# Performance work log

Measured on AMD Instinct MI355X. Metric: run time of the kernel, lower is better.

The kernel has to match this reference:

```python
import jax, jax.numpy as jnp
import numpy as np

D_MODEL = 1024
N_HEADS = 16
D_HEAD = 64
D_FF = 4096
WINDOW = 256
B, T = 2, 2048


def setup_inputs() -> dict:
    key = jax.random.key(0)
    ks = jax.random.split(key, 10)
    tot = N_HEADS * D_HEAD
    def w(k, shape):
        # approximate kaiming_normal_ fan_out init: std = sqrt(2/fan_out)
        fan_out = shape[0]
        return jax.random.normal(k, shape, jnp.float32) * np.sqrt(2.0 / fan_out)
    return {
        "x": jax.random.normal(ks[0], (B, T, D_MODEL), jnp.float32),
        "ln1_w": jnp.ones((D_MODEL,), jnp.float32),
        "qkv_w": w(ks[1], (3 * tot, D_MODEL)),
        "gate_w": w(ks[2], (tot, D_MODEL)),
        "out_w": w(ks[3], (D_MODEL, tot)),
        "ln2_w": jnp.ones((D_MODEL,), jnp.float32),
        "wg": w(ks[4], (D_FF, D_MODEL)),
        "wu": w(ks[5], (D_FF, D_MODEL)),
        "wo": w(ks[6], (D_MODEL, D_FF)),
    }


def _rmsnorm(x, w):
    return x * jax.lax.rsqrt(jnp.mean(x * x, axis=-1, keepdims=True) + 1e-6) * w


def _attention(x, qkv_w, gate_w, out_w):
    Bq, Tq, _ = x.shape
    tot = N_HEADS * D_HEAD
    qkv = x @ qkv_w.T  # [B,T,3*tot]
    q, k, v = jnp.split(qkv, 3, axis=-1)
    q = q.reshape(Bq, Tq, N_HEADS, D_HEAD).transpose(0, 2, 1, 3)
    k = k.reshape(Bq, Tq, N_HEADS, D_HEAD).transpose(0, 2, 1, 3)
    v = v.reshape(Bq, Tq, N_HEADS, D_HEAD).transpose(0, 2, 1, 3)
    scale = D_HEAD ** -0.5
    scores = jnp.einsum("bhqd,bhkd->bhqk", q, k) * scale
    pos = jnp.arange(Tq)
    dist = pos[:, None] - pos[None, :]
    allowed = (dist >= 0) & (dist < WINDOW)  # causal sliding window
    mask = jnp.where(allowed, 0.0, -jnp.inf).astype(scores.dtype)
    attn = jax.nn.softmax(scores + mask[None, None], axis=-1)
    out = jnp.einsum("bhqk,bhkd->bhqd", attn, v)
    out = out.transpose(0, 2, 1, 3).reshape(Bq, Tq, tot)
    gate = jax.nn.sigmoid(x @ gate_w.T)
    return (out * gate) @ out_w.T


def reference(x, ln1_w, qkv_w, gate_w, out_w, ln2_w, wg, wu, wo):
    x = x + _attention(_rmsnorm(x, ln1_w), qkv_w, gate_w, out_w)
    h = _rmsnorm(x, ln2_w)
    ffn = (jax.nn.silu(h @ wg.T) * (h @ wu.T)) @ wo.T
    return x + ffn
```

## Files before the change

### kernel.cpp

```cpp
#include <hip/hip_runtime.h>


#define DEV __device__ __forceinline__

using u16 = unsigned short;
typedef __attribute__((ext_vector_type(8))) short  short8;
typedef __attribute__((ext_vector_type(4))) float  floatx4;

DEV u16 f2bf(float f) {
  unsigned u = __builtin_bit_cast(unsigned, f);
  u += 0x7FFFu + ((u >> 16) & 1u);
  return (u16)(u >> 16);
}
DEV float bf2f(u16 h) {
  unsigned u = ((unsigned)h) << 16;
  return __builtin_bit_cast(float, u);
}
DEV floatx4 mfma16(short8 a, short8 b, floatx4 c) {
  return __builtin_amdgcn_mfma_f32_16x16x32_bf16(a, b, c, 0, 0, 0);
}
DEV void gload16(const u16* g, const u16* lds_base_wave_uniform) {
  __builtin_amdgcn_global_load_lds(
      (const __attribute__((address_space(1))) void*)g,
      (__attribute__((address_space(3))) void*)lds_base_wave_uniform,
      16, 0, 0);
}
#define WAITVM(n) asm volatile("s_waitcnt vmcnt(" #n ")" ::: "memory")
DEV void blockbar() {
  __builtin_amdgcn_sched_barrier(0);
  asm volatile("" ::: "memory");
  __builtin_amdgcn_s_barrier();
  asm volatile("" ::: "memory");
  __builtin_amdgcn_sched_barrier(0);
}

__global__ __launch_bounds__(256) void cvt_all_k(
    const float* __restrict__ s0, const float* __restrict__ s1,
    const float* __restrict__ s2, const float* __restrict__ s3,
    const float* __restrict__ s4, const float* __restrict__ s5,
    u16* __restrict__ d0, u16* __restrict__ d1, u16* __restrict__ d2,
    u16* __restrict__ d3, u16* __restrict__ d4, u16* __restrict__ d5) {
  const int b = blockIdx.x;
  const float* in; u16* out; int base;
  if (b < 3072)       { in = s0; out = d0; base = 0; }
  else if (b < 4096)  { in = s1; out = d1; base = 3072; }
  else if (b < 5120)  { in = s2; out = d2; base = 4096; }
  else if (b < 9216)  { in = s3; out = d3; base = 5120; }
  else if (b < 13312) { in = s4; out = d4; base = 9216; }
  else                { in = s5; out = d5; base = 13312; }
  const size_t i = (size_t)(b - base) * 256 + threadIdx.x;
  const float4 v = ((const float4*)in)[i];
  ushort4 r;
  r.x = f2bf(v.x); r.y = f2bf(v.y); r.z = f2bf(v.z); r.w = f2bf(v.w);
  ((ushort4*)out)[i] = r;
}

__global__ __launch_bounds__(256) void rmsnorm_k(const float* __restrict__ x,
                                                 const float* __restrict__ wt,
                                                 u16* __restrict__ o) {
  __shared__ float red[4];
  const int row = blockIdx.x;
  const int tid = threadIdx.x;
  const float4 v = ((const float4*)(x + (size_t)row * 1024))[tid];
  float ss = v.x * v.x + v.y * v.y + v.z * v.z + v.w * v.w;
  ss += __shfl_xor(ss, 1, 64);
  ss += __shfl_xor(ss, 2, 64);
  ss += __shfl_xor(ss, 4, 64);
  ss += __shfl_xor(ss, 8, 64);
  ss += __shfl_xor(ss, 16, 64);
  ss += __shfl_xor(ss, 32, 64);
  if ((tid & 63) == 0) red[tid >> 6] = ss;
  __syncthreads();
  const float tot = red[0] + red[1] + red[2] + red[3];
  const float sc = rsqrtf(tot * (1.0f / 1024.0f) + 1e-6f);
  const float4 wv = ((const float4*)wt)[tid];
  ushort4 r;
  r.x = f2bf(v.x * sc * wv.x);
  r.y = f2bf(v.y * sc * wv.y);
  r.z = f2bf(v.z * sc * wv.z);
  r.w = f2bf(v.w * sc * wv.w);
  ((ushort4*)(o + (size_t)row * 1024))[tid] = r;
}

template <int CFG, int EPI>
__global__ __launch_bounds__(512, 2) void gemm8w(
    const u16* __restrict__ Ag, const u16* __restrict__ Bg, int N, int K,
    u16* __restrict__ cb, float* __restrict__ cf,
    const u16* __restrict__ aux, const float* __restrict__ resid,
    u16* __restrict__ cb2) {
  constexpr int BM = (CFG == 0) ? 256 : 128;
  constexpr int TB = BM * 64;
  constexpr int CPW = TB / 1024 / 8;
  constexpr int NI = (BM / 2) / 16;
  constexpr int NJ = (BM / 4) / 16;
  __shared__ __align__(16) char lds[8 * TB];

  const int tid = threadIdx.x;
  const int w = tid >> 6, lane = tid & 63;
  const int wm = w >> 2, wn = w & 3;
  const int g = lane >> 4, r16 = lane & 15;
  const int wr0 = wm * (BM / 2), wc0 = wn * (BM / 4);

  int bid = blockIdx.y * gridDim.x + blockIdx.x;
  const int cpx = (gridDim.x * gridDim.y) >> 3;
  bid = (bid & 7) * cpx + (bid >> 3);
  const int m0 = (bid / gridDim.x) * BM;
  const int n0 = (bid % gridDim.x) * BM;

  floatx4 acc[NI][NJ];
#pragma unroll
  for (int i = 0; i < NI; i++)
#pragma unroll
    for (int j = 0; j < NJ; j++) acc[i][j] = (floatx4){0.f, 0.f, 0.f, 0.f};

  const int nk = K >> 5;
  const int xorlane = ((lane >> 3) & 7) << 4;

  auto stage = [&](int t) {
    const int bufo = (t & 3) * TB;
    const int k0 = t << 5;
#pragma unroll
    for (int q = 0; q < CPW; ++q) {
      const int c = w + (q << 3);
      const int d = (c << 10) + (lane << 4);
      const int bl = d ^ xorlane;
      const int row = ((bl >> 7) << 1) | ((bl >> 6) & 1);
      const int col = (bl & 63) >> 1;
      gload16(Ag + (size_t)(m0 + row) * K + k0 + col,
              (const u16*)(lds + bufo + (c << 10)));
      gload16(Bg + (size_t)(n0 + row) * K + k0 + col,
              (const u16*)(lds + 4 * TB + bufo + (c << 10)));
    }
  };

  stage(0); stage(1); stage(2);
  if constexpr (CFG == 0) WAITVM(8); else WAITVM(4);
  blockbar();

  const int xorr = ((r16 >> 1) & 7) << 4;
  const int baseA = ((((wr0 + r16) >> 1) << 7) + ((r16 & 1) << 6) + (g << 4)) ^ xorr;
  const int baseB = ((((wc0 + r16) >> 1) << 7) + ((r16 & 1) << 6) + (g << 4)) ^ xorr;

  for (int kt = 0; kt < nk; ++kt) {
    if (kt + 3 < nk) stage(kt + 3);
    const char* Ab = lds + (kt & 3) * TB;
    const char* Bb = lds + 4 * TB + (kt & 3) * TB;

    short8 af[NI / 2], bfv[NJ];
#pragma unroll
    for (int q = 0; q < NI / 2; q++) af[q] = *(const short8*)(Ab + baseA + (q << 10));
#pragma unroll
    for (int q = 0; q < NJ / 2; q++) bfv[q] = *(const short8*)(Bb + baseB + (q << 10));
    __builtin_amdgcn_s_setprio(1);
#pragma unroll
    for (int i = 0; i < NI / 2; i++)
#pragma unroll
      for (int j = 0; j < NJ / 2; j++) acc[i][j] = mfma16(af[i], bfv[j], acc[i][j]);
    __builtin_amdgcn_s_setprio(0);
#pragma unroll
    for (int q = NJ / 2; q < NJ; q++) bfv[q] = *(const short8*)(Bb + baseB + (q << 10));
    __builtin_amdgcn_s_setprio(1);
#pragma unroll
    for (int i = 0; i < NI / 2; i++)
#pragma unroll
      for (int j = NJ / 2; j < NJ; j++) acc[i][j] = mfma16(af[i], bfv[j], acc[i][j]);
    __builtin_amdgcn_s_setprio(0);
#pragma unroll
    for (int q = 0; q < NI / 2; q++)
      af[q] = *(const short8*)(Ab + baseA + ((NI / 2 + q) << 10));
    __builtin_amdgcn_s_setprio(1);
#pragma unroll
    for (int i = 0; i < NI / 2; i++)
#pragma unroll
      for (int j = NJ / 2; j < NJ; j++)
        acc[NI / 2 + i][j] = mfma16(af[i], bfv[j], acc[NI / 2 + i][j]);
    __builtin_amdgcn_s_setprio(0);
    __builtin_amdgcn_s_setprio(1);
#pragma unroll
    for (int i = 0; i < NI / 2; i++)
#pragma unroll
      for (int j = 0; j < NJ / 2; j++)
        acc[NI / 2 + i][j] = mfma16(af[i], bfv[j], acc[NI / 2 + i][j]);
    __builtin_amdgcn_s_setprio(0);

    if (kt + 1 < nk) {
      if (kt + 3 < nk)      { if constexpr (CFG == 0) WAITVM(8); else WAITVM(4); }
      else if (kt + 2 < nk) { if constexpr (CFG == 0) WAITVM(4); else WAITVM(2); }
      else                  { WAITVM(0); }
      blockbar();
    }
  }

#pragma unroll
  for (int i = 0; i < NI; i++) {
    const int row = m0 + wr0 + i * 16 + g * 4;
#pragma unroll
    for (int j = 0; j < NJ; j++) {
      const int col = n0 + wc0 + j * 16 + r16;
#pragma unroll
      for (int rr = 0; rr < 4; rr++) {
        const float v = acc[i][j][rr];
        if constexpr (EPI == 2) {
          cb[(size_t)(row + rr) * N + col] = f2bf(v / (1.0f + __expf(-v)));
        } else if constexpr (EPI == 3) {
          const size_t idx = (size_t)(row + rr) * N + col;
          cb[idx] = f2bf(v * bf2f(aux[idx]));
        } else if constexpr (EPI == 4) {
          const size_t idx = (size_t)(row + rr) * N + col;
          cf[idx] = v + resid[idx];
        } else if constexpr (EPI == 6) {
          if (col < 3072)
            cb[(size_t)(row + rr) * 3072 + col] = f2bf(v);
          else
            cb2[(size_t)(row + rr) * 1024 + (col - 3072)] =
                f2bf(1.0f / (1.0f + __expf(-v)));
        }
      }
    }
  }
}

__global__ __launch_bounds__(256) void attn_win_kernel(
    const u16* __restrict__ qkv, const u16* __restrict__ gate,
    u16* __restrict__ out) {
  __shared__ __align__(16) u16 Kl[64][80];
  __shared__ __align__(16) u16 Vt[64][80];
  __shared__ __align__(16) u16 Pl[4][16][80];

  const int tid = threadIdx.x;
  const int w = tid >> 6, lane = tid & 63;
  const int g = lane >> 4, r16 = lane & 15;

  const int q0 = blockIdx.x * 64;
  const int h = blockIdx.y;
  const int b = blockIdx.z;
  const u16* qb_ = qkv + (size_t)b * 2048 * 3072;

  const int tq = q0 + w * 16 + r16;
  const u16* qptr = qb_ + (size_t)tq * 3072 + h * 64;
  const short8 aq0 = *(const short8*)(qptr + g * 8);
  const short8 aq1 = *(const short8*)(qptr + 32 + g * 8);

  floatx4 O[4] = {{0,0,0,0},{0,0,0,0},{0,0,0,0},{0,0,0,0}};
  float mrow[4] = {-1e30f, -1e30f, -1e30f, -1e30f};
  float lrow[4] = {0.f, 0.f, 0.f, 0.f};

  const int srow = tid >> 2;
  const int sq4 = tid & 3;
  const int qw = q0 + w * 16;

  for (int kt = q0 - 256; kt <= q0; kt += 64) {
    if (kt < 0) continue;
    {
      const u16* kb = qb_ + (size_t)(kt + srow) * 3072 + 1024 + h * 64 + sq4 * 16;
      const short8 kv0 = *(const short8*)kb;
      const short8 kv1 = *(const short8*)(kb + 8);
      *(short8*)&Kl[srow][sq4 * 16] = kv0;
      *(short8*)&Kl[srow][sq4 * 16 + 8] = kv1;
      const u16* vb = kb + 1024;
      const short8 vv0 = *(const short8*)vb;
      const short8 vv1 = *(const short8*)(vb + 8);
#pragma unroll
      for (int j = 0; j < 8; j++) Vt[sq4 * 16 + j][srow] = (u16)vv0[j];
#pragma unroll
      for (int j = 0; j < 8; j++) Vt[sq4 * 16 + 8 + j][srow] = (u16)vv1[j];
    }
    __syncthreads();

    const bool active = (qw + 15 >= kt) && (qw - kt < 319);
    if (active) {
      floatx4 S[4];
#pragma unroll
      for (int nf = 0; nf < 4; nf++) {
        const short8 bk0 = *(const short8*)&Kl[nf * 16 + r16][g * 8];
        const short8 bk1 = *(const short8*)&Kl[nf * 16 + r16][32 + g * 8];
        floatx4 a = {0.f, 0.f, 0.f, 0.f};
        a = mfma16(aq0, bk0, a);
        a = mfma16(aq1, bk1, a);
        S[nf] = a;
      }
      float pm[4][4];
      float nmax[4] = {-1e30f, -1e30f, -1e30f, -1e30f};
#pragma unroll
      for (int nf = 0; nf < 4; nf++) {
        const int key = kt + nf * 16 + r16;
#pragma unroll
        for (int rr = 0; rr < 4; rr++) {
          const int q = qw + g * 4 + rr;
          const int dist = q - key;
          const float s = (dist >= 0 && dist < 256) ? S[nf][rr] : -1e30f;
          pm[nf][rr] = s;
          nmax[rr] = fmaxf(nmax[rr], s);
        }
      }
#pragma unroll
      for (int rr = 0; rr < 4; rr++) {
        float v = nmax[rr];
        v = fmaxf(v, __shfl_xor(v, 1, 64));
        v = fmaxf(v, __shfl_xor(v, 2, 64));
        v = fmaxf(v, __shfl_xor(v, 4, 64));
        v = fmaxf(v, __shfl_xor(v, 8, 64));
        const float mnew = fmaxf(mrow[rr], v);
        const float alpha = __expf(0.125f * (mrow[rr] - mnew));
        mrow[rr] = mnew;
        lrow[rr] *= alpha;
#pragma unroll
        for (int n = 0; n < 4; n++) O[n][rr] *= alpha;
        float ls = 0.f;
#pragma unroll
        for (int nf = 0; nf < 4; nf++) {
          const float s = pm[nf][rr];
          const float pv = (s < -1e29f) ? 0.f : __expf(0.125f * (s - mnew));
          pm[nf][rr] = pv;
          ls += pv;
        }
        ls += __shfl_xor(ls, 1, 64);
        ls += __shfl_xor(ls, 2, 64);
        ls += __shfl_xor(ls, 4, 64);
        ls += __shfl_xor(ls, 8, 64);
        lrow[rr] += ls;
      }
#pragma unroll
      for (int nf = 0; nf < 4; nf++)
#pragma unroll
        for (int rr = 0; rr < 4; rr++)
          Pl[w][g * 4 + rr][nf * 16 + r16] = f2bf(pm[nf][rr]);
#pragma unroll
      for (int kf = 0; kf < 2; kf++) {
        const short8 pa = *(const short8*)&Pl[w][r16][kf * 32 + g * 8];
#pragma unroll
        for (int n = 0; n < 4; n++) {
          const short8 vb8 = *(const short8*)&Vt[n * 16 + r16][kf * 32 + g * 8];
          O[n] = mfma16(pa, vb8, O[n]);
        }
      }
    }
    __syncthreads();
  }

#pragma unroll
  for (int n = 0; n < 4; n++) {
#pragma unroll
    for (int rr = 0; rr < 4; rr++) {
      const int t = qw + g * 4 + rr;
      const size_t idx = ((size_t)(b * 2048 + t)) * 1024 + h * 64 + n * 16 + r16;
      const float gv = bf2f(gate[idx]);
      const float ov = (O[n][rr] / lrow[rr]) * gv;
      out[idx] = f2bf(ov);
    }
  }
}

extern "C" void kernel_launch(void* const* d_in, const int* in_sizes, int n_in,
                              void* d_out, int out_size, void* d_ws,
                              size_t ws_size, hipStream_t stream) {
  (void)in_sizes; (void)n_in; (void)out_size; (void)ws_size;
  const float* x     = (const float*)d_in[0];
  const float* ln1   = (const float*)d_in[1];
  const float* qkvw  = (const float*)d_in[2];
  const float* gatew = (const float*)d_in[3];
  const float* outw  = (const float*)d_in[4];
  const float* ln2   = (const float*)d_in[5];
  const float* wg    = (const float*)d_in[6];
  const float* wu    = (const float*)d_in[7];
  const float* wo    = (const float*)d_in[8];
  float* outp = (float*)d_out;

  u16* p = (u16*)d_ws;
  u16* qkvw_b  = p; p += 3 * 1024 * 1024;
  u16* gatew_b = p; p += 1024 * 1024;
  u16* outw_b  = p; p += 1024 * 1024;
  u16* wg_b    = p; p += 4 * 1024 * 1024;
  u16* wu_b    = p; p += 4 * 1024 * 1024;
  u16* wo_b    = p; p += 4 * 1024 * 1024;
  u16* xn      = p; p += 4096 * 1024;
  u16* qkvb    = p; p += (size_t)4096 * 3072;
  u16* gates   = p; p += 4096 * 1024;
  u16* a3      = p; p += 4096 * 1024;
  u16* hb      = p; p += 4096 * 1024;
  u16* gs      = p; p += (size_t)4096 * 4096;
  float* x2    = (float*)p;

  cvt_all_k<<<17408, 256, 0, stream>>>(qkvw, gatew, outw, wg, wu, wo,
                                       qkvw_b, gatew_b, outw_b, wg_b, wu_b, wo_b);

  rmsnorm_k<<<4096, 256, 0, stream>>>(x, ln1, xn);

  gemm8w<0, 6><<<dim3(16, 16), 512, 0, stream>>>(
      xn, qkvw_b, 4096, 1024, qkvb, nullptr, nullptr, nullptr, gates);

  attn_win_kernel<<<dim3(32, 16, 2), 256, 0, stream>>>(qkvb, gates, a3);

  gemm8w<1, 4><<<dim3(8, 32), 512, 0, stream>>>(
      a3, outw_b, 1024, 1024, nullptr, x2, nullptr, x, nullptr);

  rmsnorm_k<<<4096, 256, 0, stream>>>(x2, ln2, hb);

  gemm8w<0, 2><<<dim3(16, 16), 512, 0, stream>>>(
      hb, wg_b, 4096, 1024, gs, nullptr, nullptr, nullptr, nullptr);
  gemm8w<0, 3><<<dim3(16, 16), 512, 0, stream>>>(
      hb, wu_b, 4096, 1024, gs, nullptr, gs, nullptr, nullptr);

  gemm8w<1, 4><<<dim3(8, 32), 512, 0, stream>>>(
      gs, wo_b, 1024, 4096, nullptr, outp, nullptr, x2, nullptr);
}
```

Before: 389.0 us.

## Restructure GEMM into double-buffered 64-wide K tiles with interleaved sub-stage loads

Rewrites the bf16 MFMA GEMM pipeline. The old kernel used a 4-deep ring of 32-wide K stages with XOR-swizzled LDS. The new one uses two 64-wide K buffers split into four sub-groups (A/B by K half), whose loads for the next tile are issued between the MFMA phases of the current tile. The 128-tile configuration now runs with 4 waves (256 threads) instead of 8, each wave computing a 64x64 output. The aim is to overlap global-to-LDS traffic with compute and cut barrier overhead. The risks are that dropping the XOR swizzle adds LDS bank conflicts, and that the extra in-loop barriers and fewer waves on the small GEMMs reduce latency hiding.

```diff
diff --git a/kernel.cpp b/kernel.cpp
--- a/kernel.cpp
+++ b/kernel.cpp
@@ -19,7 +19,7 @@
 DEV floatx4 mfma16(short8 a, short8 b, floatx4 c) {
   return __builtin_amdgcn_mfma_f32_16x16x32_bf16(a, b, c, 0, 0, 0);
 }
-DEV void gload16(const u16* g, const u16* lds_base_wave_uniform) {
+DEV void gload16(const u16* g, const char* lds_base_wave_uniform) {
   __builtin_amdgcn_global_load_lds(
       (const __attribute__((address_space(1))) void*)g,
       (__attribute__((address_space(3))) void*)lds_base_wave_uniform,
@@ -27,11 +27,9 @@
 }
 #define WAITVM(n) asm volatile("s_waitcnt vmcnt(" #n ")" ::: "memory")
 DEV void blockbar() {
-  __builtin_amdgcn_sched_barrier(0);
   asm volatile("" ::: "memory");
   __builtin_amdgcn_s_barrier();
   asm volatile("" ::: "memory");
-  __builtin_amdgcn_sched_barrier(0);
 }
 
 __global__ __launch_bounds__(256) void cvt_all_k(
@@ -83,23 +81,26 @@
 }
 
 template <int CFG, int EPI>
-__global__ __launch_bounds__(512, 2) void gemm8w(
+__global__ __launch_bounds__((CFG == 0) ? 512 : 256, 2) void gemm8p(
     const u16* __restrict__ Ag, const u16* __restrict__ Bg, int N, int K,
     u16* __restrict__ cb, float* __restrict__ cf,
     const u16* __restrict__ aux, const float* __restrict__ resid,
     u16* __restrict__ cb2) {
   constexpr int BM = (CFG == 0) ? 256 : 128;
-  constexpr int TB = BM * 64;
-  constexpr int CPW = TB / 1024 / 8;
-  constexpr int NI = (BM / 2) / 16;
-  constexpr int NJ = (BM / 4) / 16;
-  __shared__ __align__(16) char lds[8 * TB];
+  constexpr int NWAVES = (CFG == 0) ? 8 : 4;
+  constexpr int WAVES_N = (CFG == 0) ? 4 : 2;
+  constexpr int WM = (CFG == 0) ? 128 : 64;
+  constexpr int NI = WM / 16;
+  constexpr int NJ = 4;
+  constexpr int IH = (CFG == 0) ? NI / 2 : NI;
+  constexpr int GB = BM * 64;
+  constexpr int BUFB = 4 * GB;
+  __shared__ __align__(16) char lds[2 * BUFB];
 
   const int tid = threadIdx.x;
   const int w = tid >> 6, lane = tid & 63;
-  const int wm = w >> 2, wn = w & 3;
+  const int wm = w / WAVES_N, wn = w % WAVES_N;
   const int g = lane >> 4, r16 = lane & 15;
-  const int wr0 = wm * (BM / 2), wc0 = wn * (BM / 4);
 
   int bid = blockIdx.y * gridDim.x + blockIdx.x;
   const int cpx = (gridDim.x * gridDim.y) >> 3;
@@ -113,90 +114,90 @@
 #pragma unroll
     for (int j = 0; j < NJ; j++) acc[i][j] = (floatx4){0.f, 0.f, 0.f, 0.f};
 
-  const int nk = K >> 5;
-  const int xorlane = ((lane >> 3) & 7) << 4;
-
-  auto stage = [&](int t) {
-    const int bufo = (t & 3) * TB;
-    const int k0 = t << 5;
-#pragma unroll
-    for (int q = 0; q < CPW; ++q) {
-      const int c = w + (q << 3);
-      const int d = (c << 10) + (lane << 4);
-      const int bl = d ^ xorlane;
-      const int row = ((bl >> 7) << 1) | ((bl >> 6) & 1);
-      const int col = (bl & 63) >> 1;
-      gload16(Ag + (size_t)(m0 + row) * K + k0 + col,
-              (const u16*)(lds + bufo + (c << 10)));
-      gload16(Bg + (size_t)(n0 + row) * K + k0 + col,
-              (const u16*)(lds + 4 * TB + bufo + (c << 10)));
-    }
+  const int nt = K >> 6;
+
+  const int srow = w * 32 + (lane >> 2);
+  const int scol8 = (lane & 3) * 8;
+  auto stageG = [&](int G, int t) {
+    if (t >= nt) return;
+    const u16* Mat = (G < 2) ? Ag : Bg;
+    const int base0 = (G < 2) ? m0 : n0;
+    const int kc = t * 64 + (G & 1) * 32 + scol8;
+    const char* dst = lds + (t & 1) * BUFB + G * GB + w * 2048;
+#pragma unroll
+    for (int q = 0; q < 2; q++)
+      gload16(Mat + (size_t)(base0 + srow + q * 16) * K + kc, dst + q * 1024);
   };
 
-  stage(0); stage(1); stage(2);
-  if constexpr (CFG == 0) WAITVM(8); else WAITVM(4);
-  blockbar();
-
-  const int xorr = ((r16 >> 1) & 7) << 4;
-  const int baseA = ((((wr0 + r16) >> 1) << 7) + ((r16 & 1) << 6) + (g << 4)) ^ xorr;
-  const int baseB = ((((wc0 + r16) >> 1) << 7) + ((r16 & 1) << 6) + (g << 4)) ^ xorr;
-
-  for (int kt = 0; kt < nk; ++kt) {
-    if (kt + 3 < nk) stage(kt + 3);
-    const char* Ab = lds + (kt & 3) * TB;
-    const char* Bb = lds + 4 * TB + (kt & 3) * TB;
-
-    short8 af[NI / 2], bfv[NJ];
-#pragma unroll
-    for (int q = 0; q < NI / 2; q++) af[q] = *(const short8*)(Ab + baseA + (q << 10));
-#pragma unroll
-    for (int q = 0; q < NJ / 2; q++) bfv[q] = *(const short8*)(Bb + baseB + (q << 10));
+  auto rdA = [&](short8* af, int ks, int ihalf, const char* buf) {
+#pragma unroll
+    for (int i = 0; i < IH; i++) {
+      const int arow = wm * WM + (ihalf * IH + i) * 16 + r16;
+      af[i] = *(const short8*)(buf + ks * GB + arow * 64 + g * 16);
+    }
+  };
+  auto rdB = [&](short8* bf_, int ks, const char* buf) {
+#pragma unroll
+    for (int j = 0; j < NJ; j++) {
+      const int brow = wn * 64 + j * 16 + r16;
+      bf_[j] = *(const short8*)(buf + 2 * GB + ks * GB + brow * 64 + g * 16);
+    }
+  };
+  auto mm = [&](short8* af, short8* bf_, int ihalf) {
     __builtin_amdgcn_s_setprio(1);
 #pragma unroll
-    for (int i = 0; i < NI / 2; i++)
-#pragma unroll
-      for (int j = 0; j < NJ / 2; j++) acc[i][j] = mfma16(af[i], bfv[j], acc[i][j]);
+    for (int i = 0; i < IH; i++)
+#pragma unroll
+      for (int j = 0; j < NJ; j++)
+        acc[ihalf * IH + i][j] = mfma16(af[i], bf_[j], acc[ihalf * IH + i][j]);
     __builtin_amdgcn_s_setprio(0);
-#pragma unroll
-    for (int q = NJ / 2; q < NJ; q++) bfv[q] = *(const short8*)(Bb + baseB + (q << 10));
-    __builtin_amdgcn_s_setprio(1);
-#pragma unroll
-    for (int i = 0; i < NI / 2; i++)
-#pragma unroll
-      for (int j = NJ / 2; j < NJ; j++) acc[i][j] = mfma16(af[i], bfv[j], acc[i][j]);
-    __builtin_amdgcn_s_setprio(0);
-#pragma unroll
-    for (int q = 0; q < NI / 2; q++)
-      af[q] = *(const short8*)(Ab + baseA + ((NI / 2 + q) << 10));
-    __builtin_amdgcn_s_setprio(1);
-#pragma unroll
-    for (int i = 0; i < NI / 2; i++)
-#pragma unroll
-      for (int j = NJ / 2; j < NJ; j++)
-        acc[NI / 2 + i][j] = mfma16(af[i], bfv[j], acc[NI / 2 + i][j]);
-    __builtin_amdgcn_s_setprio(0);
-    __builtin_amdgcn_s_setprio(1);
-#pragma unroll
-    for (int i = 0; i < NI / 2; i++)
-#pragma unroll
-      for (int j = 0; j < NJ / 2; j++)
-        acc[NI / 2 + i][j] = mfma16(af[i], bfv[j], acc[NI / 2 + i][j]);
-    __builtin_amdgcn_s_setprio(0);
-
-    if (kt + 1 < nk) {
-      if (kt + 3 < nk)      { if constexpr (CFG == 0) WAITVM(8); else WAITVM(4); }
-      else if (kt + 2 < nk) { if constexpr (CFG == 0) WAITVM(4); else WAITVM(2); }
-      else                  { WAITVM(0); }
-      blockbar();
+  };
+
+  if constexpr (CFG == 0) { stageG(1, 0); stageG(2, 0); stageG(0, 0); stageG(3, 0); }
+  else                    { stageG(0, 0); stageG(2, 0); stageG(1, 0); stageG(3, 0); }
+
+  for (int t = 0; t < nt; ++t) {
+    const char* buf = lds + (t & 1) * BUFB;
+    short8 af[IH], bfv[NJ];
+    if constexpr (CFG == 0) {
+      WAITVM(2);
+      blockbar();
+      rdA(af, 0, 0, buf); rdB(bfv, 0, buf);
+      stageG(1, t + 1);
+      mm(af, bfv, 0);
+      blockbar();
+      rdA(af, 0, 1, buf);
+      stageG(2, t + 1);
+      mm(af, bfv, 1);
+      if (t + 1 < nt) { WAITVM(4); } else { WAITVM(0); }
+      blockbar();
+      rdA(af, 1, 0, buf); rdB(bfv, 1, buf);
+      stageG(0, t + 1);
+      mm(af, bfv, 0);
+      blockbar();
+      rdA(af, 1, 1, buf);
+      stageG(3, t + 1);
+      mm(af, bfv, 1);
+    } else {
+      WAITVM(4);
+      blockbar();
+      rdA(af, 0, 0, buf); rdB(bfv, 0, buf);
+      stageG(0, t + 1); stageG(2, t + 1);
+      mm(af, bfv, 0);
+      if (t + 1 < nt) { WAITVM(4); } else { WAITVM(0); }
+      blockbar();
+      rdA(af, 1, 0, buf); rdB(bfv, 1, buf);
+      stageG(1, t + 1); stageG(3, t + 1);
+      mm(af, bfv, 0);
     }
   }
 
 #pragma unroll
   for (int i = 0; i < NI; i++) {
-    const int row = m0 + wr0 + i * 16 + g * 4;
+    const int row = m0 + wm * WM + i * 16 + g * 4;
 #pragma unroll
     for (int j = 0; j < NJ; j++) {
-      const int col = n0 + wc0 + j * 16 + r16;
+      const int col = n0 + wn * 64 + j * 16 + r16;
 #pragma unroll
       for (int rr = 0; rr < 4; rr++) {
         const float v = acc[i][j][rr];
@@ -386,21 +387,21 @@
 
   rmsnorm_k<<<4096, 256, 0, stream>>>(x, ln1, xn);
 
-  gemm8w<0, 6><<<dim3(16, 16), 512, 0, stream>>>(
+  gemm8p<0, 6><<<dim3(16, 16), 512, 0, stream>>>(
       xn, qkvw_b, 4096, 1024, qkvb, nullptr, nullptr, nullptr, gates);
 
   attn_win_kernel<<<dim3(32, 16, 2), 256, 0, stream>>>(qkvb, gates, a3);
 
-  gemm8w<1, 4><<<dim3(8, 32), 512, 0, stream>>>(
+  gemm8p<1, 4><<<dim3(8, 32), 256, 0, stream>>>(
       a3, outw_b, 1024, 1024, nullptr, x2, nullptr, x, nullptr);
 
   rmsnorm_k<<<4096, 256, 0, stream>>>(x2, ln2, hb);
 
-  gemm8w<0, 2><<<dim3(16, 16), 512, 0, stream>>>(
+  gemm8p<0, 2><<<dim3(16, 16), 512, 0, stream>>>(
       hb, wg_b, 4096, 1024, gs, nullptr, nullptr, nullptr, nullptr);
-  gemm8w<0, 3><<<dim3(16, 16), 512, 0, stream>>>(
+  gemm8p<0, 3><<<dim3(16, 16), 512, 0, stream>>>(
       hb, wu_b, 4096, 1024, gs, nullptr, gs, nullptr, nullptr);
 
-  gemm8w<1, 4><<<dim3(8, 32), 512, 0, stream>>>(
+  gemm8p<1, 4><<<dim3(8, 32), 256, 0, stream>>>(
       gs, wo_b, 1024, 4096, nullptr, outp, nullptr, x2, nullptr);
 }
```

Measured after the change: 364.7 us. -6.2%, faster.
